# Kernel optimization log

Hardware: AMD Instinct MI355X
Metric: run time of the kernel (lower is better)

## Reference

```python
import jax, jax.numpy as jnp
import numpy as np


def _hann_filter(P):
    # ramp filter built in spatial domain (Kak & Slaney) times fftshifted Hann window
    n = np.concatenate([np.arange(1, P // 2 + 1, 2), np.arange(P // 2 - 1, 0, -2)]).astype(np.float64)
    f = np.zeros(P, np.float64)
    f[0] = 0.25
    f[1::2] = -1.0 / (np.pi * n) ** 2
    ramp = 2.0 * np.real(np.fft.fft(f))
    filt = ramp * np.fft.fftshift(np.hanning(P))
    return jnp.asarray(filt, jnp.float32)


def _fbp(sino, angles, circle):
    B, A, L = sino.shape
    P = max(64, int(2 ** np.ceil(np.log2(2 * L))))  # img_size_padded
    center = L // 2
    # --- FFT filtering (filtered=True) ---
    filt = _hann_filter(P)
    sino_p = jnp.pad(sino, ((0, 0), (0, 0), (0, P - L)))
    sino_f = jnp.real(jnp.fft.ifft(jnp.fft.fft(sino_p, axis=-1) * filt, axis=-1))[:, :, :L]
    # --- back-projection: emulate grid_sample(bilinear, align_corners=True, padding zeros) ---
    x, y = jnp.meshgrid(jnp.arange(L, dtype=jnp.float32) - center,
                        jnp.arange(L, dtype=jnp.float32) - center, indexing='ij')
    th = angles + jnp.pi / 2
    t = x[None] * jnp.cos(th)[:, None, None] + y[None] * jnp.sin(th)[:, None, None]  # [A,L,L]
    # t_norm = 2t/(L-1); align_corners pixel coord = (t_norm+1)/2*(L-1) = t + (L-1)/2
    u = t + (L - 1) / 2.0
    i0 = jnp.floor(u)
    frac = u - i0
    i0i = i0.astype(jnp.int32)
    i1i = i0i + 1
    v0 = (i0i >= 0) & (i0i < L)
    v1 = (i1i >= 0) & (i1i < L)
    w0 = jnp.where(v0, 1.0 - frac, 0.0)  # zero-padding: kill OOB taps
    w1 = jnp.where(v1, frac, 0.0)
    aidx = jnp.arange(A)[:, None, None]
    g0 = sino_f[:, aidx, jnp.clip(i0i, 0, L - 1)]  # [B,A,L,L]
    g1 = sino_f[:, aidx, jnp.clip(i1i, 0, L - 1)]
    recon = jnp.sum(w0[None] * g0 + w1[None] * g1, axis=1)  # [B,L,L]
    if circle:
        Y, X = np.ogrid[:L, :L]
        mask = jnp.asarray(np.sqrt((X - center) ** 2 + (Y - center) ** 2) > center)
        recon = jnp.where(mask[None], 0.0, recon)
    return recon


def setup_inputs() -> dict:
    key = jax.random.key(0)
    sino = jax.random.normal(key, (2, 181, 512), dtype=jnp.float32)
    angles = jnp.linspace(0.0, np.pi, 181).astype(jnp.float32)
    return {"sino": sino, "angles": angles, "circle": 1}


def reference(sino, angles, circle):
    return _fbp(sino, angles, circle)
```

## Files before the change

### kernel.cpp

```cpp
#include <hip/hip_runtime.h>
#include <math.h>

#define OFF_FILT 0
#define OFF_HR   1024
#define OFF_CTH  2048
#define OFF_STH  2304
#define OFF_SF   4096
#define OFF_P    189440
#define WS_NEED  (2286592ull * 4ull)

__device__ __forceinline__ float cos2pi(float x) {
  return __builtin_amdgcn_cosf(x);
}

__global__ __launch_bounds__(256) void k_filt(const float* __restrict__ angles,
                                              float* __restrict__ ws,
                                              float* __restrict__ out) {
  const int t = threadIdx.x & 63;
  const int k = blockIdx.x * 4 + (threadIdx.x >> 6);
  float acc = 0.f;
#pragma unroll
  for (int q = 0; q < 8; q++) {
    int tt = t + 64 * q;
    int n = (tt < 256) ? (2 * tt + 1) : (1023 - 2 * tt);
    float pin = 3.14159265358979f * (float)n;
    float cf = -1.0f / (pin * pin);
    int r = ((2 * tt + 1) * k) & 1023;
    acc = fmaf(cf, cos2pi((float)r * (1.0f / 1024.0f)), acc);
  }
#pragma unroll
  for (int o = 32; o; o >>= 1) acc += __shfl_down(acc, o, 64);
  if (t == 0) {
    float ramp = 0.5f + 2.0f * acc;
    int ks = (k + 512) & 1023;
    float hann = 0.5f - 0.5f * cos2pi((float)ks * (1.0f / 1023.0f));
    ws[OFF_FILT + k] = ramp * hann;
  }
  if (blockIdx.x == 0 && threadIdx.x < 181) {
    float th = angles[threadIdx.x] + 1.5707963267948966f;
    ws[OFF_CTH + threadIdx.x] = cosf(th);
    ws[OFF_STH + threadIdx.x] = sinf(th);
  }
  const float4 z4 = make_float4(0.f, 0.f, 0.f, 0.f);
  float4* o4 = (float4*)out;
  int idx = blockIdx.x * 256 + threadIdx.x;
  o4[idx] = z4;
  o4[idx + 65536] = z4;
}

__global__ __launch_bounds__(256) void k_hr(float* __restrict__ ws) {
  const int t = threadIdx.x & 63;
  const int m = blockIdx.x * 4 + (threadIdx.x >> 6);
  float acc = 0.f;
  int r = (t * m) & 1023;
  const int step = (64 * m) & 1023;
#pragma unroll
  for (int q = 0; q < 16; q++) {
    acc = fmaf(ws[OFF_FILT + t + 64 * q],
               cos2pi((float)r * (1.0f / 1024.0f)), acc);
    r = (r + step) & 1023;
  }
#pragma unroll
  for (int o = 32; o; o >>= 1) acc += __shfl_down(acc, o, 64);
  if (t == 0) ws[OFF_HR + m] = acc * (1.0f / 1024.0f);
}

__global__ __launch_bounds__(64) void k_conv(const float* __restrict__ sino,
                                             float* __restrict__ ws) {
  __shared__ float s_s0[512];
  __shared__ float s_s1[512];
  __shared__ float s_hr[1024];
  const int t = threadIdx.x;
  const int a = blockIdx.x;
  const float4* r0 = (const float4*)(sino + (size_t)a * 512);
  const float4* r1 = (const float4*)(sino + (size_t)(181 + a) * 512);
  ((float4*)s_s0)[t] = r0[t];
  ((float4*)s_s0)[t + 64] = r0[t + 64];
  ((float4*)s_s1)[t] = r1[t];
  ((float4*)s_s1)[t + 64] = r1[t + 64];
  const float4* hr4 = (const float4*)(ws + OFF_HR);
#pragma unroll
  for (int q = 0; q < 4; q++) ((float4*)s_hr)[t + 64 * q] = hr4[t + 64 * q];
  __syncthreads();

  const int base = blockIdx.y * 256 + t * 4;
  float acc0[4] = {0.f, 0.f, 0.f, 0.f};
  float acc1[4] = {0.f, 0.f, 0.f, 0.f};
  const float4* SH = (const float4*)s_hr;
  const float4* S0 = (const float4*)s_s0;
  const float4* S1 = (const float4*)s_s1;
  for (int j8 = 0; j8 < 512; j8 += 8) {
    float4 sa0 = S0[j8 >> 2];
    float4 sb0 = S0[(j8 >> 2) + 1];
    float4 sa1 = S1[j8 >> 2];
    float4 sb1 = S1[(j8 >> 2) + 1];
    int w = base - j8;
    float4 h0 = SH[((w - 8) & 1023) >> 2];
    float4 h1 = SH[((w - 4) & 1023) >> 2];
    float4 h2 = SH[(w & 1023) >> 2];
    float qq[12] = {h0.x, h0.y, h0.z, h0.w, h1.x, h1.y,
                    h1.z, h1.w, h2.x, h2.y, h2.z, h2.w};
    float v0[8] = {sa0.x, sa0.y, sa0.z, sa0.w, sb0.x, sb0.y, sb0.z, sb0.w};
    float v1[8] = {sa1.x, sa1.y, sa1.z, sa1.w, sb1.x, sb1.y, sb1.z, sb1.w};
#pragma unroll
    for (int jj = 0; jj < 8; jj++) {
#pragma unroll
      for (int m = 0; m < 4; m++) {
        acc0[m] = fmaf(v0[jj], qq[8 + m - jj], acc0[m]);
        acc1[m] = fmaf(v1[jj], qq[8 + m - jj], acc1[m]);
      }
    }
  }
  float* dst = ws + OFF_SF + (size_t)a * 1024 + base * 2;
  ((float4*)dst)[0] = make_float4(acc0[0], acc1[0], acc0[1], acc1[1]);
  ((float4*)dst)[1] = make_float4(acc0[2], acc1[2], acc0[3], acc1[3]);
}

#define PAD   108
#define ROWE  728
#define CHUNK 4
__global__ __launch_bounds__(512) void k_bp(const float* __restrict__ ws,
                                            const int* __restrict__ circ,
                                            float* __restrict__ pbuf,
                                            float* __restrict__ out,
                                            int mode) {
  __shared__ float2 srow[CHUNK * ROWE];
  const int j = threadIdx.x;
  const int i0 = blockIdx.x * 2;
  const int by = blockIdx.y;
  const int abase = (by * 181) >> 2;
  const int aend = ((by + 1) * 181) >> 2;
  const float xc = (float)(i0 - 256);
  const float yc = (float)(j - 256);
  const float* __restrict__ cth = ws + OFF_CTH;
  const float* __restrict__ sth = ws + OFF_STH;
  float a00 = 0.f, a01 = 0.f, a10 = 0.f, a11 = 0.f;

  const float2 z2 = make_float2(0.f, 0.f);
#pragma unroll
  for (int r = 0; r < CHUNK; r++) {
    if (j < PAD) srow[r * ROWE + j] = z2;
    if (j < ROWE - PAD - 512) srow[r * ROWE + PAD + 512 + j] = z2;
  }

  const int rb = j >> 8;
  const int col = j & 255;
  const float4* __restrict__ G = (const float4*)(ws + OFF_SF);
  const int rowcap = aend - 1;
  float4* SW0 = (float4*)&srow[rb * ROWE + PAD + 2 * col];
  float4* SW1 = (float4*)&srow[(rb + 2) * ROWE + PAD + 2 * col];

  int A = abase;
  float4 pre0 = G[min(A + rb, rowcap) * 256 + col];
  float4 pre1 = G[min(A + rb + 2, rowcap) * 256 + col];

  for (int c = 0; c < 12; c++) {
    __syncthreads();
    *SW0 = pre0;
    *SW1 = pre1;
    const int An = A + CHUNK;
    if (c < 11) {
      pre0 = G[min(An + rb, rowcap) * 256 + col];
      pre1 = G[min(An + rb + 2, rowcap) * 256 + col];
    }
    __syncthreads();
    const int nv = min(CHUNK, aend - A);
#pragma unroll
    for (int r = 0; r < CHUNK; r++) {
      if (r >= nv) break;
      const int a = A + r;
      const float c_ = cth[a];
      const float s_ = sth[a];
      float u0 = fmaf(xc, c_, fmaf(yc, s_, 255.5f + (float)PAD));
      float u1 = u0 + c_;
      float fl0 = floorf(u0), fl1 = floorf(u1);
      float fr0 = u0 - fl0, fr1 = u1 - fl1;
      int b0 = (int)fl0, b1 = (int)fl1;
      const float2* rp = &srow[r * ROWE];
      float2 p00 = rp[b0];
      float2 p01 = rp[b0 + 1];
      float2 p10 = rp[b1];
      float2 p11 = rp[b1 + 1];
      float w0 = 1.0f - fr0, w1 = 1.0f - fr1;
      a00 = fmaf(w0, p00.x, fmaf(fr0, p01.x, a00));
      a01 = fmaf(w0, p00.y, fmaf(fr0, p01.y, a01));
      a10 = fmaf(w1, p10.x, fmaf(fr1, p11.x, a10));
      a11 = fmaf(w1, p10.y, fmaf(fr1, p11.y, a11));
    }
    A = An;
  }

  const size_t o0 = (size_t)i0 * 512 + j;
  if (mode == 0) {
    float* pb = pbuf + (size_t)by * 524288;
    pb[o0] = a00;
    pb[262144 + o0] = a01;
    pb[o0 + 512] = a10;
    pb[262144 + o0 + 512] = a11;
  } else {
    const int dx = j - 256;
    const bool con = (circ[0] != 0);
    const int dy0 = i0 - 256, dy1 = i0 + 1 - 256;
    if (!(con && dx * dx + dy0 * dy0 > 65536)) {
      atomicAdd(&out[o0], a00);
      atomicAdd(&out[262144 + o0], a01);
    }
    if (!(con && dx * dx + dy1 * dy1 > 65536)) {
      atomicAdd(&out[o0 + 512], a10);
      atomicAdd(&out[262144 + o0 + 512], a11);
    }
  }
}

__global__ __launch_bounds__(256) void k_sum(const float* __restrict__ ws,
                                             const int* __restrict__ circ,
                                             float* __restrict__ out) {
  const int idx = blockIdx.x * 256 + threadIdx.x;
  const float4* P0 = (const float4*)(ws + OFF_P);
  const float4* P1 = P0 + 131072;
  const float4* P2 = P1 + 131072;
  const float4* P3 = P2 + 131072;
  float4 v0 = P0[idx], v1 = P1[idx], v2 = P2[idx], v3 = P3[idx];
  float4 v = make_float4(v0.x + v1.x + v2.x + v3.x,
                         v0.y + v1.y + v2.y + v3.y,
                         v0.z + v1.z + v2.z + v3.z,
                         v0.w + v1.w + v2.w + v3.w);
  if (circ[0] != 0) {
    const int f = (idx * 4) & 262143;
    const int ii = f >> 9;
    const int jj = f & 511;
    const int dy = ii - 256;
    const int dyy = dy * dy;
    const int d0 = jj - 256;
    if (d0 * d0 + dyy > 65536) v.x = 0.f;
    if ((d0 + 1) * (d0 + 1) + dyy > 65536) v.y = 0.f;
    if ((d0 + 2) * (d0 + 2) + dyy > 65536) v.z = 0.f;
    if ((d0 + 3) * (d0 + 3) + dyy > 65536) v.w = 0.f;
  }
  ((float4*)out)[idx] = v;
}

extern "C" void kernel_launch(void* const* d_in, const int* in_sizes, int n_in,
                              void* d_out, int out_size, void* d_ws, size_t ws_size,
                              hipStream_t stream) {
  const float* sino = (const float*)d_in[0];
  const float* angles = (const float*)d_in[1];
  const int* circ = (const int*)d_in[2];
  float* ws = (float*)d_ws;
  float* out = (float*)d_out;
  const int partial = (ws_size >= WS_NEED) ? 1 : 0;

  hipLaunchKernelGGL(k_filt, dim3(256),    dim3(256), 0, stream, angles, ws, out);
  hipLaunchKernelGGL(k_hr,   dim3(256),    dim3(256), 0, stream, ws);
  hipLaunchKernelGGL(k_conv, dim3(181, 2), dim3(64),  0, stream, sino, ws);
  if (partial) {
    hipLaunchKernelGGL(k_bp,  dim3(256, 4), dim3(512), 0, stream,
                       ws, circ, ws + OFF_P, out, 0);
    hipLaunchKernelGGL(k_sum, dim3(512),    dim3(256), 0, stream, ws, circ, out);
  } else {
    hipLaunchKernelGGL(k_bp,  dim3(256, 4), dim3(512), 0, stream,
                       ws, circ, ws + OFF_P, out, 1);
  }
}
```

Measured before the change: 96.63 us.

## Store filtered sinogram as packed fp16 pairs and double back-projection angle chunk

The filter kernel now writes each filtered sinogram sample pair (both batches) as a packed half2 instead of two floats, halving its storage and the global/LDS traffic of the back-projection. The back-projection kernel stages 8 angles per chunk in LDS (same LDS bytes), halving the number of barrier-separated iterations, and converts the halves to float before interpolation. This cuts memory traffic and synchronisation but lowers the precision of the intermediate data to fp16, which may break tolerance.

```diff
diff --git a/kernel.cpp b/kernel.cpp
--- a/kernel.cpp
+++ b/kernel.cpp
@@ -1,4 +1,5 @@
 #include <hip/hip_runtime.h>
+#include <hip/hip_fp16.h>
 #include <math.h>
 
 #define OFF_FILT 0
@@ -11,6 +12,18 @@
 
 __device__ __forceinline__ float cos2pi(float x) {
   return __builtin_amdgcn_cosf(x);
+}
+
+__device__ __forceinline__ unsigned pkh2(float x, float y) {
+  __half2 h = __halves2half2(__float2half_rn(x), __float2half_rn(y));
+  unsigned u;
+  __builtin_memcpy(&u, &h, 4);
+  return u;
+}
+__device__ __forceinline__ float2 uph2(unsigned u) {
+  __half2 h;
+  __builtin_memcpy(&h, &u, 4);
+  return __half22float2(h);
 }
 
 __global__ __launch_bounds__(256) void k_filt(const float* __restrict__ angles,
@@ -111,20 +124,21 @@
       }
     }
   }
-  float* dst = ws + OFF_SF + (size_t)a * 1024 + base * 2;
-  ((float4*)dst)[0] = make_float4(acc0[0], acc1[0], acc0[1], acc1[1]);
-  ((float4*)dst)[1] = make_float4(acc0[2], acc1[2], acc0[3], acc1[3]);
+  unsigned* dstu = (unsigned*)(ws + OFF_SF) + (size_t)a * 512 + base;
+  uint4 pk = make_uint4(pkh2(acc0[0], acc1[0]), pkh2(acc0[1], acc1[1]),
+                        pkh2(acc0[2], acc1[2]), pkh2(acc0[3], acc1[3]));
+  *(uint4*)dstu = pk;
 }
 
 #define PAD   108
 #define ROWE  728
-#define CHUNK 4
-__global__ __launch_bounds__(512) void k_bp(const float* __restrict__ ws,
-                                            const int* __restrict__ circ,
-                                            float* __restrict__ pbuf,
-                                            float* __restrict__ out,
-                                            int mode) {
-  __shared__ float2 srow[CHUNK * ROWE];
+#define CHUNK 8
+__global__ __launch_bounds__(512, 8) void k_bp(const float* __restrict__ ws,
+                                               const int* __restrict__ circ,
+                                               float* __restrict__ pbuf,
+                                               float* __restrict__ out,
+                                               int mode) {
+  __shared__ unsigned srow[CHUNK * ROWE];
   const int j = threadIdx.x;
   const int i0 = blockIdx.x * 2;
   const int by = blockIdx.y;
@@ -136,32 +150,33 @@
   const float* __restrict__ sth = ws + OFF_STH;
   float a00 = 0.f, a01 = 0.f, a10 = 0.f, a11 = 0.f;
 
-  const float2 z2 = make_float2(0.f, 0.f);
 #pragma unroll
   for (int r = 0; r < CHUNK; r++) {
-    if (j < PAD) srow[r * ROWE + j] = z2;
-    if (j < ROWE - PAD - 512) srow[r * ROWE + PAD + 512 + j] = z2;
+    if (j < PAD) srow[r * ROWE + j] = 0u;
+    if (j < ROWE - PAD - 512) srow[r * ROWE + PAD + 512 + j] = 0u;
   }
 
   const int rb = j >> 8;
   const int col = j & 255;
-  const float4* __restrict__ G = (const float4*)(ws + OFF_SF);
+  const uint2* __restrict__ G = (const uint2*)((const unsigned*)(ws + OFF_SF));
   const int rowcap = aend - 1;
-  float4* SW0 = (float4*)&srow[rb * ROWE + PAD + 2 * col];
-  float4* SW1 = (float4*)&srow[(rb + 2) * ROWE + PAD + 2 * col];
 
   int A = abase;
-  float4 pre0 = G[min(A + rb, rowcap) * 256 + col];
-  float4 pre1 = G[min(A + rb + 2, rowcap) * 256 + col];
-
-  for (int c = 0; c < 12; c++) {
+  uint2 pre[4];
+#pragma unroll
+  for (int q = 0; q < 4; q++)
+    pre[q] = G[min(A + rb + 2 * q, rowcap) * 256 + col];
+
+  for (int c = 0; c < 6; c++) {
     __syncthreads();
-    *SW0 = pre0;
-    *SW1 = pre1;
+#pragma unroll
+    for (int q = 0; q < 4; q++)
+      *(uint2*)&srow[(rb + 2 * q) * ROWE + PAD + 2 * col] = pre[q];
     const int An = A + CHUNK;
-    if (c < 11) {
-      pre0 = G[min(An + rb, rowcap) * 256 + col];
-      pre1 = G[min(An + rb + 2, rowcap) * 256 + col];
+    if (c < 5) {
+#pragma unroll
+      for (int q = 0; q < 4; q++)
+        pre[q] = G[min(An + rb + 2 * q, rowcap) * 256 + col];
     }
     __syncthreads();
     const int nv = min(CHUNK, aend - A);
@@ -176,16 +191,16 @@
       float fl0 = floorf(u0), fl1 = floorf(u1);
       float fr0 = u0 - fl0, fr1 = u1 - fl1;
       int b0 = (int)fl0, b1 = (int)fl1;
-      const float2* rp = &srow[r * ROWE];
-      float2 p00 = rp[b0];
-      float2 p01 = rp[b0 + 1];
-      float2 p10 = rp[b1];
-      float2 p11 = rp[b1 + 1];
+      const unsigned* rp = &srow[r * ROWE];
+      unsigned qa0 = rp[b0], qb0 = rp[b0 + 1];
+      unsigned qa1 = rp[b1], qb1 = rp[b1 + 1];
+      float2 fa0 = uph2(qa0), fb0 = uph2(qb0);
+      float2 fa1 = uph2(qa1), fb1 = uph2(qb1);
       float w0 = 1.0f - fr0, w1 = 1.0f - fr1;
-      a00 = fmaf(w0, p00.x, fmaf(fr0, p01.x, a00));
-      a01 = fmaf(w0, p00.y, fmaf(fr0, p01.y, a01));
-      a10 = fmaf(w1, p10.x, fmaf(fr1, p11.x, a10));
-      a11 = fmaf(w1, p10.y, fmaf(fr1, p11.y, a11));
+      a00 = fmaf(w0, fa0.x, fmaf(fr0, fb0.x, a00));
+      a01 = fmaf(w0, fa0.y, fmaf(fr0, fb0.y, a01));
+      a10 = fmaf(w1, fa1.x, fmaf(fr1, fb1.x, a10));
+      a11 = fmaf(w1, fa1.y, fmaf(fr1, fb1.y, a11));
     }
     A = An;
   }
```

Result: no change. 98.27 us (+1.7%).
